# Kernel tuning notes

Hardware: AMD Instinct MI355X
Metric: run time of the kernel (lower is better)

The kernel has to match this reference:

```python
import jax, jax.numpy as jnp
import numpy as np
from jax import lax

NUM_SKETCH = 3
BN_EPS = 1e-5


def setup_inputs() -> dict:
    key = jax.random.key(0)
    ks = jax.random.split(key, 8)
    B, C, H, W = 32, 128, 64, 64
    D = C // 4  # comp_rate = 4
    k = 3
    x = jax.random.normal(ks[0], (B, C, H, W), dtype=jnp.float32)
    fan = C * k * k
    w1 = jax.random.normal(ks[1], (C, C, k, k), dtype=jnp.float32) / np.sqrt(fan)
    w2 = jax.random.normal(ks[2], (C, C, k, k), dtype=jnp.float32) / np.sqrt(fan)
    gamma1 = jnp.ones((C,), jnp.float32); beta1 = jnp.zeros((C,), jnp.float32)
    gamma2 = jnp.ones((C,), jnp.float32); beta2 = jnp.zeros((C,), jnp.float32)
    # count-sketch hash matrices: hs[j] is (D, C), each column c has a single 1
    idx = jax.random.randint(ks[3], (NUM_SKETCH, C), 0, D)
    hs = jax.nn.one_hot(idx, D, dtype=jnp.float32).transpose(0, 2, 1)  # (3, D, C)
    ss = (jax.random.randint(ks[4], (NUM_SKETCH, C), 0, 2) * 2 - 1).astype(jnp.float32)  # (3, C) signs
    return {"x": x, "w1": w1, "w2": w2, "gamma1": gamma1, "beta1": beta1,
            "gamma2": gamma2, "beta2": beta2, "hs": hs, "ss": ss}


def _sketch_conv_unsketch(x, w, hs, ss):
    # w: (Co, Ci, k, k); hs: (J, D, Co); ss: (J, Co)
    Co, Ci, k, _ = w.shape
    J, D, _ = hs.shape
    B, _, H, W = x.shape
    wf = w.reshape(Co, -1)  # (Co, M)
    # sketched weights per sketch j: h_j @ (wf * s_j[:, None])
    w_sk = jnp.einsum('jdc,jc,cm->jdm', hs, ss, wf).reshape(J * D, Ci, k, k)
    # one conv with J*D output channels (padding=1, stride=1 hardcoded in source)
    y = lax.conv_general_dilated(x, w_sk, window_strides=(1, 1),
                                 padding=[(1, 1), (1, 1)],
                                 dimension_numbers=('NCHW', 'OIHW', 'NCHW'))
    y = y.reshape(B, J, D, H, W)
    # unsketch activations: h_j^T @ y_j, then sign scale (num_s=1 so inner median is identity)
    y_un = jnp.einsum('jdc,bjdhw->jbchw', hs, y) * ss[:, None, :, None, None]
    return jnp.median(y_un, axis=0)  # median over the 3 sketches -> (B, Co, H, W)


def _bn_relu(y, gamma, beta):
    # BatchNorm2d in training mode: biased batch stats over (N, H, W)
    mean = jnp.mean(y, axis=(0, 2, 3), keepdims=True)
    var = jnp.var(y, axis=(0, 2, 3), keepdims=True)
    yhat = (y - mean) * lax.rsqrt(var + BN_EPS)
    return jax.nn.relu(yhat * gamma[None, :, None, None] + beta[None, :, None, None])


def reference(x, w1, w2, gamma1, beta1, gamma2, beta2, hs, ss):
    residual = x
    out1 = _bn_relu(_sketch_conv_unsketch(x, w1, hs, ss), gamma1, beta1)
    del out1  # faithful to source bug: second conv loop uses x, discarding out1
    out = _bn_relu(_sketch_conv_unsketch(x, w2, hs, ss), gamma2, beta2)
    return out + residual
```

## Files before the change

kernel.cpp:

```cpp
#include <hip/hip_runtime.h>
#include <stdint.h>

typedef __bf16 bf16x8 __attribute__((ext_vector_type(8)));
typedef float  f32x4  __attribute__((ext_vector_type(4)));

static constexpr int Bn = 32, Cn = 128, Hn = 64, Wn = 64, HWn = 4096;
static constexpr size_t OFF_XT    = 0;
static constexpr size_t OFF_WF    = 33554432;
static constexpr size_t OFF_IDX   = 33775616;
static constexpr size_t OFF_M     = 33777152;
static constexpr size_t OFF_STATS = 67331584;

__device__ __forceinline__ unsigned short f32_to_bf16(float f) {
    union { float f; unsigned u; } v; v.f = f;
    unsigned u = v.u;
    return (unsigned short)((u + 0x7FFFu + ((u >> 16) & 1u)) >> 16);
}
__device__ __forceinline__ float bf16_to_f32(unsigned short h) {
    union { unsigned u; float f; } v; v.u = ((unsigned)h) << 16;
    return v.f;
}
__device__ __forceinline__ float bf_lo(unsigned w) {
    union { unsigned u; float f; } v; v.u = w << 16; return v.f;
}
__device__ __forceinline__ float bf_hi(unsigned w) {
    union { unsigned u; float f; } v; v.u = w & 0xffff0000u; return v.f;
}
__device__ __forceinline__ float med3(float z0, float z1, float z2) {
    float lo = fminf(z0, z1), hi = fmaxf(z0, z1);
    return fmaxf(lo, fminf(hi, z2));
}

__global__ __launch_bounds__(256) void k_prep(const float* __restrict__ x,
                                              unsigned short* __restrict__ xT,
                                              const float* __restrict__ w2,
                                              const float* __restrict__ hs,
                                              const float* __restrict__ ss,
                                              unsigned short* __restrict__ wf,
                                              int* __restrict__ idx,
                                              float* __restrict__ stats16) {
    int t = threadIdx.x;
    if (blockIdx.x < 2048) {
        __shared__ __align__(16) unsigned short sm[256 * 40];
        int blk = blockIdx.x;
        int pt = blk & 15, q = (blk >> 4) & 3, b = blk >> 6;
        int p0 = pt * 256;
        const float* xp = x + ((size_t)(b * Cn + q * 32) * HWn) + p0 + t;
#pragma unroll
        for (int cil = 0; cil < 32; ++cil)
            sm[t * 40 + cil] = f32_to_bf16(xp[(size_t)cil * HWn]);
        __syncthreads();
        uint4* dst = (uint4*)(xT + ((size_t)(b * 4 + q) * HWn + p0) * 32);
#pragma unroll
        for (int pass = 0; pass < 4; ++pass) {
            int pix = pass * 64 + (t >> 2);
            int ch  = t & 3;
            dst[pix * 4 + ch] = *(const uint4*)(&sm[pix * 40 + ch * 8]);
        }
    } else if (blockIdx.x < 2480) {
        int f = (blockIdx.x - 2048) * 256 + t;
        int jj   = f & 7;
        int lane = (f >> 3) & 63;
        int nt   = (f >> 9) % 6;
        int qt   = f / (512 * 6);
        int tp   = qt % 9;
        int q    = qt / 9;
        int k  = ((lane >> 4) << 3) + jj;
        int ci = q * 32 + k;
        int n  = nt * 16 + (lane & 15);
        int j = n >> 5, d = n & 31;
        float sum = 0.f;
        for (int c = 0; c < 128; ++c) {
            float g = hs[(j * 32 + d) * 128 + c];
            if (g != 0.f) sum += g * ss[j * 128 + c] * w2[(c * 128 + ci) * 9 + tp];
        }
        wf[f] = f32_to_bf16(sum);
    } else {
        for (int i = t; i < 384; i += 256) {
            int j = i >> 7, c = i & 127;
            int found = 0;
            for (int d = 0; d < 32; ++d)
                if (hs[(j * 32 + d) * 128 + c] > 0.5f) found = d;
            idx[i] = found;
        }
        for (int i = t; i < 4096; i += 256) stats16[i] = 0.f;
    }
}

__global__ __launch_bounds__(256, 2) void k_conv(const unsigned short* __restrict__ xT,
                                                 const unsigned short* __restrict__ wf,
                                                 const int* __restrict__ idx,
                                                 const float* __restrict__ ss,
                                                 unsigned short* __restrict__ m_out,
                                                 float* __restrict__ stats16) {
    __shared__ __align__(16) unsigned short sm[25344];
    __shared__ int   idx_sh[384];
    __shared__ float ss_sh[384];
    int tid  = threadIdx.x;
    int blk  = blockIdx.x;
    int tile = blk & 15, b = blk >> 4;
    int ty0  = tile * 4;
    int wv   = tid >> 6, lane = tid & 63;
    int quad = lane >> 4, l15 = lane & 15;

    for (int i = tid; i < 384; i += 256) { idx_sh[i] = idx[i]; ss_sh[i] = ss[i]; }

    f32x4 acc[4][6];
#pragma unroll
    for (int a = 0; a < 4; ++a)
#pragma unroll
        for (int nb = 0; nb < 6; ++nb) acc[a][nb] = (f32x4){0.f, 0.f, 0.f, 0.f};

    const unsigned short* wl = wf + lane * 8;

    for (int q = 0; q < 4; ++q) {
        __syncthreads();
#pragma unroll
        for (int pass = 0; pass < 2; ++pass) {
            int r = tid + pass * 256;
            if (r < 396) {
                int hy = r / 66, hx = r - hy * 66;
                int gy = ty0 + hy - 1, gx = hx - 1;
                uint4* dst = (uint4*)(&sm[r * 40]);
                if (gy >= 0 && gy < 64 && gx >= 0 && gx < 64) {
                    const uint4* src = (const uint4*)(xT + ((size_t)(b * 4 + q) * HWn + gy * 64 + gx) * 32);
                    dst[0] = src[0]; dst[1] = src[1]; dst[2] = src[2]; dst[3] = src[3];
                } else {
                    uint4 z = {0u, 0u, 0u, 0u};
                    dst[0] = z; dst[1] = z; dst[2] = z; dst[3] = z;
                }
            }
        }
        __syncthreads();
#pragma unroll
        for (int tp = 0; tp < 9; ++tp) {
            int dy = tp / 3, dx = tp % 3;
            bf16x8 bfr[6];
            const unsigned short* wb = wl + (size_t)((q * 9 + tp) * 6) * 512;
#pragma unroll
            for (int nb = 0; nb < 6; ++nb)
                bfr[nb] = *(const bf16x8*)(wb + nb * 512);
            bf16x8 afr[4];
#pragma unroll
            for (int mq = 0; mq < 4; ++mq) {
                int off = ((wv + dy) * 66 + mq * 16 + l15 + dx) * 40 + quad * 8;
                afr[mq] = *(const bf16x8*)(&sm[off]);
            }
#pragma unroll
            for (int mq = 0; mq < 4; ++mq)
#pragma unroll
                for (int nb = 0; nb < 6; ++nb)
                    acc[mq][nb] = __builtin_amdgcn_mfma_f32_16x16x32_bf16(afr[mq], bfr[nb], acc[mq][nb], 0, 0, 0);
        }
    }
    __syncthreads();
#pragma unroll
    for (int mq = 0; mq < 4; ++mq)
#pragma unroll
        for (int nb = 0; nb < 6; ++nb) {
            int ch = nb * 16 + l15;
            int px = wv * 64 + mq * 16 + quad * 4;
            ushort4 v;
            v.x = f32_to_bf16(acc[mq][nb][0]);
            v.y = f32_to_bf16(acc[mq][nb][1]);
            v.z = f32_to_bf16(acc[mq][nb][2]);
            v.w = f32_to_bf16(acc[mq][nb][3]);
            *(ushort4*)(&sm[ch * 264 + px]) = v;
        }
    __syncthreads();
    int half = lane >> 5, p8 = lane & 31;
    unsigned short* mpb = m_out + (size_t)b * Cn * HWn + tile * 256 + p8 * 8;
    float* stp = stats16 + (blk & 15) * 256;
#pragma unroll 2
    for (int i = 0; i < 16; ++i) {
        int c = wv * 32 + i * 2 + half;
        int r0 = idx_sh[c], r1 = 32 + idx_sh[128 + c], r2 = 64 + idx_sh[256 + c];
        float sg0 = ss_sh[c], sg1 = ss_sh[128 + c], sg2 = ss_sh[256 + c];
        uint4 w0 = *(const uint4*)(&sm[r0 * 264 + p8 * 8]);
        uint4 w1 = *(const uint4*)(&sm[r1 * 264 + p8 * 8]);
        uint4 w2v = *(const uint4*)(&sm[r2 * 264 + p8 * 8]);
        const unsigned* u0 = (const unsigned*)&w0;
        const unsigned* u1 = (const unsigned*)&w1;
        const unsigned* u2 = (const unsigned*)&w2v;
        uint4 R;
        unsigned* rw = (unsigned*)&R;
        float s = 0.f, s2 = 0.f;
#pragma unroll
        for (int e = 0; e < 4; ++e) {
            float mlo = med3(sg0 * bf_lo(u0[e]), sg1 * bf_lo(u1[e]), sg2 * bf_lo(u2[e]));
            float mhi = med3(sg0 * bf_hi(u0[e]), sg1 * bf_hi(u1[e]), sg2 * bf_hi(u2[e]));
            s  += mlo + mhi;
            s2 += mlo * mlo + mhi * mhi;
            rw[e] = (unsigned)f32_to_bf16(mlo) | ((unsigned)f32_to_bf16(mhi) << 16);
        }
        *(uint4*)(mpb + (size_t)c * HWn) = R;
#pragma unroll
        for (int o = 16; o > 0; o >>= 1) { s += __shfl_xor(s, o); s2 += __shfl_xor(s2, o); }
        if ((lane & 31) == 0) { atomicAdd(&stp[c], s); atomicAdd(&stp[128 + c], s2); }
    }
}

__global__ __launch_bounds__(256) void k_apply(const unsigned short* __restrict__ m,
                                               const float* __restrict__ x,
                                               const float* __restrict__ stats16,
                                               const float* __restrict__ gamma,
                                               const float* __restrict__ beta,
                                               float* __restrict__ out) {
    int i4 = blockIdx.x * 256 + threadIdx.x;
    size_t base = (size_t)i4 * 4;
    int c = (int)((base >> 12) & 127);
    float S = 0.f, S2 = 0.f;
#pragma unroll
    for (int k = 0; k < 16; ++k) {
        S  += stats16[k * 256 + c];
        S2 += stats16[k * 256 + 128 + c];
    }
    const float N = 131072.f;
    float mean = S / N;
    float var  = S2 / N - mean * mean;
    float sc   = gamma[c] * rsqrtf(var + 1e-5f);
    float sh   = beta[c] - mean * sc;
    ushort4 mv = ((const ushort4*)m)[i4];
    float4  xv = ((const float4*)x)[i4];
    float4 o;
    o.x = fmaxf(bf16_to_f32(mv.x) * sc + sh, 0.f) + xv.x;
    o.y = fmaxf(bf16_to_f32(mv.y) * sc + sh, 0.f) + xv.y;
    o.z = fmaxf(bf16_to_f32(mv.z) * sc + sh, 0.f) + xv.z;
    o.w = fmaxf(bf16_to_f32(mv.w) * sc + sh, 0.f) + xv.w;
    ((float4*)out)[i4] = o;
}

extern "C" void kernel_launch(void* const* d_in, const int* in_sizes, int n_in,
                              void* d_out, int out_size, void* d_ws, size_t ws_size,
                              hipStream_t stream) {
    const float* x      = (const float*)d_in[0];
    const float* w2     = (const float*)d_in[2];
    const float* gamma2 = (const float*)d_in[5];
    const float* beta2  = (const float*)d_in[6];
    const float* hs     = (const float*)d_in[7];
    const float* ss     = (const float*)d_in[8];
    float* out = (float*)d_out;

    char* ws = (char*)d_ws;
    unsigned short* xT  = (unsigned short*)(ws + OFF_XT);
    unsigned short* wfp = (unsigned short*)(ws + OFF_WF);
    int*            idp = (int*)(ws + OFF_IDX);
    unsigned short* mp  = (unsigned short*)(ws + OFF_M);
    float*          st  = (float*)(ws + OFF_STATS);

    k_prep<<<2481, 256, 0, stream>>>(x, xT, w2, hs, ss, wfp, idp, st);
    k_conv<<<512, 256, 0, stream>>>(xT, wfp, idp, ss, mp, st);
    k_apply<<<16384, 256, 0, stream>>>(mp, x, st, gamma2, beta2, out);
}
```

Before: 205.9 us.

## Double-buffer conv input tiles via direct global-to-LDS loads with swizzled layout

```diff
diff --git a/kernel.cpp b/kernel.cpp
--- a/kernel.cpp
+++ b/kernel.cpp
@@ -10,6 +10,7 @@
 static constexpr size_t OFF_IDX   = 33775616;
 static constexpr size_t OFF_M     = 33777152;
 static constexpr size_t OFF_STATS = 67331584;
+static constexpr size_t OFF_ZERO  = 67347968;
 
 __device__ __forceinline__ unsigned short f32_to_bf16(float f) {
     union { float f; unsigned u; } v; v.f = f;
@@ -29,6 +30,12 @@
 __device__ __forceinline__ float med3(float z0, float z1, float z2) {
     float lo = fminf(z0, z1), hi = fmaxf(z0, z1);
     return fmaxf(lo, fminf(hi, z2));
+}
+__device__ __forceinline__ void gload_lds16(const unsigned short* g, unsigned short* l) {
+    __builtin_amdgcn_global_load_lds(
+        (const __attribute__((address_space(1))) unsigned int*)(const void*)g,
+        (__attribute__((address_space(3))) unsigned int*)(void*)l,
+        16, 0, 0);
 }
 
 __global__ __launch_bounds__(256) void k_prep(const float* __restrict__ x,
@@ -38,27 +45,24 @@
                                               const float* __restrict__ ss,
                                               unsigned short* __restrict__ wf,
                                               int* __restrict__ idx,
-                                              float* __restrict__ stats16) {
+                                              float* __restrict__ stats16,
+                                              float* __restrict__ zerop) {
+    __shared__ __align__(16) unsigned char smraw[20480];
     int t = threadIdx.x;
-    if (blockIdx.x < 2048) {
-        __shared__ __align__(16) unsigned short sm[256 * 40];
-        int blk = blockIdx.x;
-        int pt = blk & 15, q = (blk >> 4) & 3, b = blk >> 6;
-        int p0 = pt * 256;
-        const float* xp = x + ((size_t)(b * Cn + q * 32) * HWn) + p0 + t;
-#pragma unroll
-        for (int cil = 0; cil < 32; ++cil)
-            sm[t * 40 + cil] = f32_to_bf16(xp[(size_t)cil * HWn]);
+    if (blockIdx.x < 432) {
+        int*   idxs = (int*)smraw;
+        float* sss  = (float*)(smraw + 1536);
+        for (int i = t; i < 384; i += 256) {
+            int j = i >> 7, c = i & 127;
+            int found = 0;
+#pragma unroll
+            for (int d = 0; d < 32; ++d)
+                if (hs[(j * 32 + d) * 128 + c] > 0.5f) found = d;
+            idxs[i] = found;
+            sss[i]  = ss[i];
+        }
         __syncthreads();
-        uint4* dst = (uint4*)(xT + ((size_t)(b * 4 + q) * HWn + p0) * 32);
-#pragma unroll
-        for (int pass = 0; pass < 4; ++pass) {
-            int pix = pass * 64 + (t >> 2);
-            int ch  = t & 3;
-            dst[pix * 4 + ch] = *(const uint4*)(&sm[pix * 40 + ch * 8]);
-        }
-    } else if (blockIdx.x < 2480) {
-        int f = (blockIdx.x - 2048) * 256 + t;
+        int f = blockIdx.x * 256 + t;
         int jj   = f & 7;
         int lane = (f >> 3) & 63;
         int nt   = (f >> 9) % 6;
@@ -69,13 +73,13 @@
         int ci = q * 32 + k;
         int n  = nt * 16 + (lane & 15);
         int j = n >> 5, d = n & 31;
+        const int*   ij = idxs + j * 128;
+        const float* sj = sss  + j * 128;
         float sum = 0.f;
-        for (int c = 0; c < 128; ++c) {
-            float g = hs[(j * 32 + d) * 128 + c];
-            if (g != 0.f) sum += g * ss[j * 128 + c] * w2[(c * 128 + ci) * 9 + tp];
-        }
+        for (int c = 0; c < 128; ++c)
+            if (ij[c] == d) sum += sj[c] * w2[(c * 128 + ci) * 9 + tp];
         wf[f] = f32_to_bf16(sum);
-    } else {
+    } else if (blockIdx.x == 432) {
         for (int i = t; i < 384; i += 256) {
             int j = i >> 7, c = i & 127;
             int found = 0;
@@ -84,6 +88,24 @@
             idx[i] = found;
         }
         for (int i = t; i < 4096; i += 256) stats16[i] = 0.f;
+        if (t < 32) zerop[t] = 0.f;
+    } else {
+        unsigned short* sm = (unsigned short*)smraw;
+        int blk = blockIdx.x - 433;
+        int pt = blk & 15, q = (blk >> 4) & 3, b = blk >> 6;
+        int p0 = pt * 256;
+        const float* xp = x + ((size_t)(b * Cn + q * 32) * HWn) + p0 + t;
+#pragma unroll
+        for (int cil = 0; cil < 32; ++cil)
+            sm[t * 40 + cil] = f32_to_bf16(xp[(size_t)cil * HWn]);
+        __syncthreads();
+        uint4* dst = (uint4*)(xT + ((size_t)(b * 4 + q) * HWn + p0) * 32);
+#pragma unroll
+        for (int pass = 0; pass < 4; ++pass) {
+            int pix = pass * 64 + (t >> 2);
+            int ch  = t & 3;
+            dst[pix * 4 + ch] = *(const uint4*)(&sm[pix * 40 + ch * 8]);
+        }
     }
 }
 
@@ -92,7 +114,8 @@
                                                  const int* __restrict__ idx,
                                                  const float* __restrict__ ss,
                                                  unsigned short* __restrict__ m_out,
-                                                 float* __restrict__ stats16) {
+                                                 float* __restrict__ stats16,
+                                                 const unsigned short* __restrict__ zerop) {
     __shared__ __align__(16) unsigned short sm[25344];
     __shared__ int   idx_sh[384];
     __shared__ float ss_sh[384];
@@ -105,6 +128,19 @@
 
     for (int i = tid; i < 384; i += 256) { idx_sh[i] = idx[i]; ss_sh[i] = ss[i]; }
 
+    int goff[7];
+#pragma unroll
+    for (int i = 0; i < 7; ++i) {
+        int k = (i < 6) ? (tid + i * 256) : (tid + 1536);
+        bool act = (i < 6) || (tid < 48);
+        int r  = k >> 2;
+        int cl = (k & 3) ^ ((r >> 1) & 3);
+        int hy = r / 66, hx = r - hy * 66;
+        int gy = ty0 + hy - 1, gx = hx - 1;
+        goff[i] = (act && gy >= 0 && gy < 64 && gx >= 0 && gx < 64)
+                ? ((gy * 64 + gx) * 32 + cl * 8) : -1;
+    }
+
     f32x4 acc[4][6];
 #pragma unroll
     for (int a = 0; a < 4; ++a)
@@ -113,25 +149,35 @@
 
     const unsigned short* wl = wf + lane * 8;
 
+    {
+        const unsigned short* xq = xT + (size_t)(b * 4) * (HWn * 32);
+#pragma unroll
+        for (int i = 0; i < 6; ++i) {
+            int k = tid + i * 256;
+            gload_lds16((goff[i] >= 0) ? (xq + goff[i]) : zerop, &sm[k * 8]);
+        }
+        if (tid < 48) {
+            int k = tid + 1536;
+            gload_lds16((goff[6] >= 0) ? (xq + goff[6]) : zerop, &sm[k * 8]);
+        }
+    }
+    __syncthreads();
+
     for (int q = 0; q < 4; ++q) {
-        __syncthreads();
-#pragma unroll
-        for (int pass = 0; pass < 2; ++pass) {
-            int r = tid + pass * 256;
-            if (r < 396) {
-                int hy = r / 66, hx = r - hy * 66;
-                int gy = ty0 + hy - 1, gx = hx - 1;
-                uint4* dst = (uint4*)(&sm[r * 40]);
-                if (gy >= 0 && gy < 64 && gx >= 0 && gx < 64) {
-                    const uint4* src = (const uint4*)(xT + ((size_t)(b * 4 + q) * HWn + gy * 64 + gx) * 32);
-                    dst[0] = src[0]; dst[1] = src[1]; dst[2] = src[2]; dst[3] = src[3];
-                } else {
-                    uint4 z = {0u, 0u, 0u, 0u};
-                    dst[0] = z; dst[1] = z; dst[2] = z; dst[3] = z;
-                }
+        unsigned short* cur = sm + (q & 1) * 12672;
+        if (q < 3) {
+            const unsigned short* xq = xT + (size_t)(b * 4 + q + 1) * (HWn * 32);
+            unsigned short* nxt = sm + ((q + 1) & 1) * 12672;
+#pragma unroll
+            for (int i = 0; i < 6; ++i) {
+                int k = tid + i * 256;
+                gload_lds16((goff[i] >= 0) ? (xq + goff[i]) : zerop, &nxt[k * 8]);
             }
-        }
-        __syncthreads();
+            if (tid < 48) {
+                int k = tid + 1536;
+                gload_lds16((goff[6] >= 0) ? (xq + goff[6]) : zerop, &nxt[k * 8]);
+            }
+        }
 #pragma unroll
         for (int tp = 0; tp < 9; ++tp) {
             int dy = tp / 3, dx = tp % 3;
@@ -143,8 +189,10 @@
             bf16x8 afr[4];
 #pragma unroll
             for (int mq = 0; mq < 4; ++mq) {
-                int off = ((wv + dy) * 66 + mq * 16 + l15 + dx) * 40 + quad * 8;
-                afr[mq] = *(const bf16x8*)(&sm[off]);
+                int pix = (wv + dy) * 66 + mq * 16 + l15 + dx;
+                int byo = (pix << 6) + (quad << 4);
+                byo ^= ((byo >> 7) & 3) << 4;
+                afr[mq] = *(const bf16x8*)((const unsigned char*)cur + byo);
             }
 #pragma unroll
             for (int mq = 0; mq < 4; ++mq)
@@ -152,8 +200,9 @@
                 for (int nb = 0; nb < 6; ++nb)
                     acc[mq][nb] = __builtin_amdgcn_mfma_f32_16x16x32_bf16(afr[mq], bfr[nb], acc[mq][nb], 0, 0, 0);
         }
-    }
-    __syncthreads();
+        __syncthreads();
+    }
+
 #pragma unroll
     for (int mq = 0; mq < 4; ++mq)
 #pragma unroll
@@ -206,18 +255,20 @@
                                                const float* __restrict__ gamma,
                                                const float* __restrict__ beta,
                                                float* __restrict__ out) {
-    int i4 = blockIdx.x * 256 + threadIdx.x;
-    size_t base = (size_t)i4 * 4;
-    int c = (int)((base >> 12) & 127);
-    float S = 0.f, S2 = 0.f;
-#pragma unroll
-    for (int k = 0; k < 16; ++k) {
-        S  += stats16[k * 256 + c];
-        S2 += stats16[k * 256 + 128 + c];
-    }
+    __shared__ float co[2];
+    int tid = threadIdx.x;
+    int i4 = blockIdx.x * 256 + tid;
+    int c = (blockIdx.x >> 2) & 127;
+    if (tid < 32) {
+        float v = stats16[(tid & 15) * 256 + ((tid >> 4) << 7) + c];
+#pragma unroll
+        for (int o = 8; o > 0; o >>= 1) v += __shfl_xor(v, o);
+        if ((tid & 15) == 0) co[tid >> 4] = v;
+    }
+    __syncthreads();
     const float N = 131072.f;
-    float mean = S / N;
-    float var  = S2 / N - mean * mean;
+    float mean = co[0] / N;
+    float var  = co[1] / N - mean * mean;
     float sc   = gamma[c] * rsqrtf(var + 1e-5f);
     float sh   = beta[c] - mean * sc;
     ushort4 mv = ((const ushort4*)m)[i4];
@@ -247,8 +298,9 @@
     int*            idp = (int*)(ws + OFF_IDX);
     unsigned short* mp  = (unsigned short*)(ws + OFF_M);
     float*          st  = (float*)(ws + OFF_STATS);
-
-    k_prep<<<2481, 256, 0, stream>>>(x, xT, w2, hs, ss, wfp, idp, st);
-    k_conv<<<512, 256, 0, stream>>>(xT, wfp, idp, ss, mp, st);
+    float*          zp  = (float*)(ws + OFF_ZERO);
+
+    k_prep<<<2481, 256, 0, stream>>>(x, xT, w2, hs, ss, wfp, idp, st, zp);
+    k_conv<<<512, 256, 0, stream>>>(xT, wfp, idp, ss, mp, st, (const unsigned short*)zp);
     k_apply<<<16384, 256, 0, stream>>>(mp, x, st, gamma2, beta2, out);
 }
```

Result: faster. 191.9 us (-6.8%).
